# Kernel optimization log

Hardware: AMD Instinct MI355X
Metric: run time of the kernel (lower is better)

The kernel has to match this reference:

```python
import jax, jax.numpy as jnp
import numpy as np

N = 768                       # atoms
E = N * (N - 1)               # complete directed graph edges
DIM = 64                      # hidden dim
CUT = 5.0                     # rbf high
NC = 50                       # n_centers = ceil(5/0.1)
ODIM = 1                      # output_dim
NCONV = 3
_centers_np = np.linspace(0.0, CUT, NC)
CENTERS = jnp.asarray(_centers_np, jnp.float32)
GAP = float(_centers_np[1] - _centers_np[0])
RO_IN = 2 * ODIM + NC         # readout input: 2*output_dim + rbf fan_out = 52


def softplus_bt(x, beta, thr):
    # torch.nn.Softplus(beta, threshold): linear above threshold
    bx = beta * x
    return jnp.where(bx > thr, x, jax.nn.softplus(bx) / beta)


def rbf(d):
    # exp(-(1/gap) * (d - mu_k)^2); d: (..., 1) -> (..., NC)
    return jnp.exp((-1.0 / GAP) * (d - CENTERS) ** 2)


def setup_inputs() -> dict:
    key = jax.random.key(0)
    ks = jax.random.split(key, 24)
    atom_types = jax.random.randint(ks[0], (N,), 0, 100)
    edge_distances = jax.random.uniform(ks[1], (E, 1), jnp.float32) * CUT
    # complete directed graph, edge order matches the nested i,j loop (i!=j)
    ii = np.repeat(np.arange(N), N)
    jj = np.tile(np.arange(N), N)
    m = ii != jj
    src = jnp.asarray(ii[m], jnp.int32)
    dst = jnp.asarray(jj[m], jnp.int32)

    def p(k, shape, fan):
        return jax.random.normal(k, shape, jnp.float32) / np.sqrt(fan)

    embedding = p(ks[2], (100, DIM), DIM).at[0].set(0.0)  # padding_idx=0
    L = NCONV
    return {
        'atom_types': atom_types, 'edge_distances': edge_distances,
        'src': src, 'dst': dst, 'embedding': embedding,
        'w1': p(ks[3], (L, DIM, DIM), DIM),                 # node_layer1 (no bias)
        'pw1': p(ks[4], (L, NC, DIM), NC), 'pb1': p(ks[5], (L, DIM), NC),
        'pw2': p(ks[6], (L, DIM, DIM), DIM), 'pb2': p(ks[7], (L, DIM), DIM),
        'qw1': p(ks[8], (L, DIM, DIM), DIM), 'qb1': p(ks[9], (L, DIM), DIM),
        'qw2': p(ks[10], (L, DIM, DIM), DIM), 'qb2': p(ks[11], (L, DIM), DIM),
        'au_w1': p(ks[12], (DIM, 64), DIM), 'au_b1': p(ks[13], (64,), DIM),
        'au_w2': p(ks[14], (64, ODIM), 64), 'au_b2': p(ks[15], (ODIM,), 64),
        'ro_w1': p(ks[16], (RO_IN, 64), RO_IN), 'ro_b1': p(ks[17], (64,), RO_IN),
        'ro_w2': p(ks[18], (64, 2), 64), 'ro_b2': p(ks[19], (2,), 64),
    }


def reference(atom_types, edge_distances, src, dst, embedding,
              w1, pw1, pb1, pw2, pb2, qw1, qb1, qw2, qb2,
              au_w1, au_b1, au_w2, au_b2, ro_w1, ro_b1, ro_w2, ro_b2):
    h = embedding[atom_types]                       # (N, DIM)
    rbf_out = rbf(edge_distances)                   # (E, NC)
    for l in range(NCONV):
        nw = h @ w1[l]                              # node weights (N, DIM)
        e = softplus_bt(rbf_out @ pw1[l] + pb1[l], 0.5, 14) @ pw2[l] + pb2[l]  # (E, DIM)
        msg = nw[src] * e                           # gather-mul (E, DIM)
        agg = jax.ops.segment_sum(msg, dst, num_segments=N)  # scatter-sum (N, DIM)
        upd = softplus_bt(agg @ qw1[l] + qb1[l], 0.5, 14) @ qw2[l] + qb2[l]
        h = h + upd
    # atom_update with ShiftSoftplus (beta=1, shift=2, threshold=20)
    ha = softplus_bt(h @ au_w1 + au_b1, 1.0, 20) - jnp.log(jnp.float32(2.0))
    ha = ha @ au_w2 + au_b2                         # (N, ODIM)
    # readout over all ordered pairs i!=j, in edge order == (src, dst)
    edge_feat = jnp.concatenate([ha[src], ha[dst], rbf_out], axis=-1)  # (E, 52)
    logits = jax.nn.relu(edge_feat @ ro_w1 + ro_b1) @ ro_w2 + ro_b2    # (E, 2)
    return jax.nn.softmax(logits, axis=-1)
```

## Files before the change

### kernel.cpp

```cpp
#include <hip/hip_runtime.h>
#include <hip/hip_fp16.h>

#define NATOMS 768
#define NM1    767
#define NEDGE  (768*767)
#define DIM    64
#define NC     50
#define GAPF   (5.0f/49.0f)
#define NIGAP  (-49.0f/5.0f)
#define G      512
#define STEPF  (5.0f/511.0f)
#define INVSTEP (511.0f/5.0f)
#define LN2F   0.693147180559945f

#define WS_H     0
#define WS_NWA   49152
#define WS_NWB   73728
#define WS_HA    98304
#define WS_DISTT 99328
#define WS_TT    689152

__device__ __forceinline__ float softplus05(float x) {
    float bx = 0.5f * x;
    return (bx > 14.0f) ? x : 2.0f * __logf(1.0f + __expf(bx));
}
__device__ __forceinline__ int lane_bcast_i(int v, int l) {
    return __builtin_amdgcn_readlane(v, l);
}
__device__ __forceinline__ float lane_bcast_f(float v, int l) {
    return __uint_as_float((unsigned)__builtin_amdgcn_readlane((int)__float_as_uint(v), l));
}
__device__ __forceinline__ float2 pair2f(unsigned p) {
    __half2 h = *reinterpret_cast<__half2*>(&p);
    return __half22float2(h);
}

__global__ __launch_bounds__(256)
void k_pre(const int* __restrict__ types, const float* __restrict__ dist,
           const float* __restrict__ emb, const float* __restrict__ w1all,
           const float* __restrict__ pw1, const float* __restrict__ pb1,
           const float* __restrict__ pw2, const float* __restrict__ pb2,
           const float* __restrict__ row1, const float* __restrict__ rob1,
           float* __restrict__ ws) {
    __shared__ float s_t[4 * 64];
    __shared__ float s_tile[64][65];
    const int tid = threadIdx.x, widx = tid >> 6, c = tid & 63;
    float*  h     = ws + WS_H;
    __half* nwh   = (__half*)(ws + WS_NWA);
    float*  distT = ws + WS_DISTT;
    __half* TTh   = (__half*)(ws + WS_TT);
    const int b = blockIdx.x;

    if (b < 512) {
        const int w = b * 4 + widx, tbl = w >> 9, g = w & 511;
        const float d = g * STEPF;
        float val;
        if (tbl < 3) {
            const float* W1 = pw1 + tbl * NC * DIM;
            float t1 = pb1[tbl * DIM + c];
            for (int k = 0; k < NC; ++k) {
                float x = d - GAPF * (float)k;
                t1 = fmaf(__expf(NIGAP * x * x), W1[k * DIM + c], t1);
            }
            s_t[widx * 64 + c] = softplus05(t1);
            const float* W2 = pw2 + tbl * DIM * DIM;
            val = pb2[tbl * DIM + c];
            #pragma unroll 8
            for (int k = 0; k < DIM; ++k)
                val = fmaf(s_t[widx * 64 + k], W2[k * DIM + c], val);
        } else {
            val = rob1[c];
            for (int k = 0; k < NC; ++k) {
                float x = d - GAPF * (float)k;
                val = fmaf(__expf(NIGAP * x * x), row1[(2 + k) * DIM + c], val);
            }
        }
        __half* TTt = TTh + tbl * (G * DIM * 2);
        TTt[(g * DIM + c) * 2] = __float2half(val);
        if (g > 0) TTt[((g - 1) * DIM + c) * 2 + 1] = __float2half(val);
    } else if (b < 704) {
        const int i = (b - 512) * 4 + widx;
        float hv = emb[types[i] * DIM + c];
        h[i * DIM + c] = hv;
        s_t[widx * 64 + c] = hv;
        float acc = 0.0f;
        #pragma unroll 8
        for (int k = 0; k < DIM; ++k)
            acc = fmaf(s_t[widx * 64 + k], w1all[k * DIM + c], acc);
        nwh[i * 64 + c] = __float2half(acc);
    } else {
        const int t = b - 704;
        const int I0 = (t / 12) * 64, J0 = (t % 12) * 64;
        #pragma unroll 4
        for (int r = 0; r < 16; ++r) {
            const int i = I0 + widx * 16 + r;
            const int j = J0 + c;
            s_tile[widx * 16 + r][c] =
                (i == j) ? 0.0f : dist[i * NM1 + (j - (j > i))];
        }
        __syncthreads();
        #pragma unroll 4
        for (int r = 0; r < 16; ++r) {
            const int j = J0 + widx * 16 + r;
            const int i = I0 + c;
            distT[j * NATOMS + i] = s_tile[c][widx * 16 + r];
        }
    }
}

__global__ __launch_bounds__(512)
void k_edgeupd(const __half2* __restrict__ TTl, const float* __restrict__ distT,
               const __half* __restrict__ nwin,
               const float* __restrict__ qw1, const float* __restrict__ qb1,
               const float* __restrict__ qw2, const float* __restrict__ qb2,
               float* __restrict__ h,
               const float* __restrict__ wnext, __half* __restrict__ nwout,
               const float* __restrict__ auw1, const float* __restrict__ aub1,
               const float* __restrict__ auw2, const float* __restrict__ aub2,
               float* __restrict__ ha, int last) {
    __shared__ float s_part[8][64];
    __shared__ float s_upd[192];
    const int tid = threadIdx.x, widx = tid >> 6, c = tid & 63;
    const int j = blockIdx.x;
    const int s0 = widx * 96;
    const int half = c >> 5, cl = c & 31;

    const char* TTrow = (const char*)TTl + cl * 8;
    float2 csum = make_float2(0.0f, 0.0f);
    {
        float d = distT[j * NATOMS + s0 + c];
        float pos = d * INVSTEP;
        int g = (int)pos;
        g = (g < 0) ? 0 : ((g > 510) ? 510 : g);
        float f = pos - (float)g;
        int kx = g * 256;
        const char* nwrow = (const char*)nwin + s0 * 128 + half * 128 + cl * 4;
        for (int grp = 0; grp < 4; ++grp) {
            uint2 st[8]; unsigned sn[8];
            #pragma unroll
            for (int u = 0; u < 8; ++u) {
                const int t = grp * 8 + u;
                int kx0 = lane_bcast_i(kx, 2 * t);
                int kx1 = lane_bcast_i(kx, 2 * t + 1);
                int kxs = half ? kx1 : kx0;
                st[u] = *(const uint2*)(TTrow + kxs);
                sn[u] = *(const unsigned*)(nwrow + t * 256);
            }
            #pragma unroll
            for (int u = 0; u < 8; ++u) {
                const int t = grp * 8 + u;
                float f0 = lane_bcast_f(f, 2 * t);
                float f1 = lane_bcast_f(f, 2 * t + 1);
                float fs = half ? f1 : f0;
                float2 ta = pair2f(st[u].x);
                float2 tb = pair2f(st[u].y);
                float2 nwf = pair2f(sn[u]);
                float e0 = fmaf(fs, ta.y - ta.x, ta.x);
                float e1 = fmaf(fs, tb.y - tb.x, tb.x);
                csum.x = fmaf(e0, nwf.x, csum.x);
                csum.y = fmaf(e1, nwf.y, csum.y);
            }
        }
    }
    {
        float d = distT[j * NATOMS + s0 + 64 + cl];
        float pos = d * INVSTEP;
        int g = (int)pos;
        g = (g < 0) ? 0 : ((g > 510) ? 510 : g);
        float f = pos - (float)g;
        int kx = g * 256;
        const char* nwrow = (const char*)nwin + (s0 + 64) * 128 + half * 128 + cl * 4;
        for (int grp = 0; grp < 2; ++grp) {
            uint2 st[8]; unsigned sn[8];
            #pragma unroll
            for (int u = 0; u < 8; ++u) {
                const int t = grp * 8 + u;
                int kx0 = lane_bcast_i(kx, 2 * t);
                int kx1 = lane_bcast_i(kx, 2 * t + 1);
                int kxs = half ? kx1 : kx0;
                st[u] = *(const uint2*)(TTrow + kxs);
                sn[u] = *(const unsigned*)(nwrow + t * 256);
            }
            #pragma unroll
            for (int u = 0; u < 8; ++u) {
                const int t = grp * 8 + u;
                float f0 = lane_bcast_f(f, 2 * t);
                float f1 = lane_bcast_f(f, 2 * t + 1);
                float fs = half ? f1 : f0;
                float2 ta = pair2f(st[u].x);
                float2 tb = pair2f(st[u].y);
                float2 nwf = pair2f(sn[u]);
                float e0 = fmaf(fs, ta.y - ta.x, ta.x);
                float e1 = fmaf(fs, tb.y - tb.x, tb.x);
                csum.x = fmaf(e0, nwf.x, csum.x);
                csum.y = fmaf(e1, nwf.y, csum.y);
            }
        }
    }
    float2 tot2;
    tot2.x = csum.x + __shfl_xor(csum.x, 32, 64);
    tot2.y = csum.y + __shfl_xor(csum.y, 32, 64);
    if (half == 0) *(float2*)&s_part[widx][2 * cl] = tot2;
    __syncthreads();

    if (widx == 0) {
        float tot = 0.0f;
        #pragma unroll
        for (int w8 = 0; w8 < 8; ++w8) tot += s_part[w8][c];
        float2 t0 = pair2f(((const unsigned*)TTl)[c]);
        float nwj = __half2float(nwin[j * 64 + c]);
        tot -= t0.x * nwj;
        s_upd[c] = tot;
        float t = qb1[c];
        #pragma unroll 8
        for (int k = 0; k < DIM; ++k) t = fmaf(s_upd[k], qw1[k * DIM + c], t);
        s_upd[64 + c] = softplus05(t);
        float o = qb2[c];
        #pragma unroll 8
        for (int k = 0; k < DIM; ++k) o = fmaf(s_upd[64 + k], qw2[k * DIM + c], o);
        float hn = h[j * DIM + c] + o;
        h[j * DIM + c] = hn;
        s_upd[128 + c] = hn;
        if (!last) {
            float v = 0.0f;
            #pragma unroll 8
            for (int k = 0; k < DIM; ++k) v = fmaf(s_upd[128 + k], wnext[k * DIM + c], v);
            nwout[j * 64 + c] = __float2half(v);
        } else {
            float t2 = aub1[c];
            #pragma unroll 8
            for (int k = 0; k < DIM; ++k) t2 = fmaf(s_upd[128 + k], auw1[k * DIM + c], t2);
            t2 = ((t2 > 20.0f) ? t2 : __logf(1.0f + __expf(t2))) - LN2F;
            float v = t2 * auw2[c];
            #pragma unroll
            for (int s = 32; s > 0; s >>= 1) v += __shfl_down(v, s, 64);
            if (c == 0) ha[j] = v + aub2[0];
        }
    }
}

__global__ __launch_bounds__(256)
void k_ro(const float* __restrict__ dist, const float* __restrict__ ha,
          const __half2* __restrict__ TTro,
          const float* __restrict__ row1, const float* __restrict__ row2,
          const float* __restrict__ rob2, float* __restrict__ out) {
    __shared__ float s_h[4][16 * 65];
    __shared__ float s_w2[128];
    const int tid = threadIdx.x, widx = tid >> 6, c = tid & 63;
    if (tid < 128) s_w2[tid] = row2[tid];
    __syncthreads();
    const int ebase = (blockIdx.x * 4 + widx) * 64;

    int kxv; float ff, fa, fb;
    {
        int eg = ebase + c;
        float d = dist[eg];
        float pos = d * INVSTEP;
        int kk = (int)pos;
        kk = (kk < 0) ? 0 : ((kk > 510) ? 510 : kk);
        kxv = kk * 256;
        ff = pos - (float)kk;
        unsigned i = (unsigned)(((unsigned long long)(unsigned)eg * 2867044662ull) >> 41);
        int r = eg - (int)i * 767;
        int jd = r + (r >= (int)i);
        fa = ha[i];
        fb = ha[jd];
    }
    const char* TTb2 = (const char*)TTro + c * 4;
    const float wa = row1[c], wb = row1[DIM + c];
    const int e2 = (c >> 1) & 15, p2 = c & 1, kh = c >> 5;
    const float bias2 = (kh == 0) ? rob2[p2] : 0.0f;
    float* sh = s_h[widx];
    #pragma unroll
    for (int ch = 0; ch < 4; ++ch) {
        #pragma unroll
        for (int half = 0; half < 2; ++half) {
            unsigned st[8];
            #pragma unroll
            for (int u = 0; u < 8; ++u) {
                const int le = ch * 16 + half * 8 + u;
                int kxu = lane_bcast_i(kxv, le);
                st[u] = *(const unsigned*)(TTb2 + kxu);
            }
            #pragma unroll
            for (int u = 0; u < 8; ++u) {
                const int le = ch * 16 + half * 8 + u;
                const int e = half * 8 + u;
                float fu  = lane_bcast_f(ff, le);
                float fau = lane_bcast_f(fa, le);
                float fbu = lane_bcast_f(fb, le);
                float2 tt = pair2f(st[u]);
                float hv = fmaf(fu, tt.y - tt.x, tt.x);
                hv = fmaf(fau, wa, hv);
                hv = fmaf(fbu, wb, hv);
                sh[e * 65 + c] = fmaxf(hv, 0.0f);
            }
        }
        float lsum = bias2;
        #pragma unroll 8
        for (int k8 = 0; k8 < 32; ++k8) {
            int k = kh * 32 + k8;
            lsum = fmaf(sh[e2 * 65 + k], s_w2[2 * k + p2], lsum);
        }
        lsum += __shfl_xor(lsum, 32, 64);
        float other = __shfl_xor(lsum, 1, 64);
        float m = fmaxf(lsum, other);
        float ea = __expf(lsum - m), eb = __expf(other - m);
        float r = ea / (ea + eb);
        if (c < 32) out[ebase * 2 + ch * 32 + c] = r;
    }
}

extern "C" void kernel_launch(void* const* d_in, const int* in_sizes, int n_in,
                              void* d_out, int out_size, void* d_ws, size_t ws_size,
                              hipStream_t stream) {
    const int*   types = (const int*)d_in[0];
    const float* dist  = (const float*)d_in[1];
    const float* emb   = (const float*)d_in[4];
    const float* w1    = (const float*)d_in[5];
    const float* pw1   = (const float*)d_in[6];
    const float* pb1   = (const float*)d_in[7];
    const float* pw2   = (const float*)d_in[8];
    const float* pb2   = (const float*)d_in[9];
    const float* qw1   = (const float*)d_in[10];
    const float* qb1   = (const float*)d_in[11];
    const float* qw2   = (const float*)d_in[12];
    const float* qb2   = (const float*)d_in[13];
    const float* auw1  = (const float*)d_in[14];
    const float* aub1  = (const float*)d_in[15];
    const float* auw2  = (const float*)d_in[16];
    const float* aub2  = (const float*)d_in[17];
    const float* row1  = (const float*)d_in[18];
    const float* rob1  = (const float*)d_in[19];
    const float* row2  = (const float*)d_in[20];
    const float* rob2  = (const float*)d_in[21];

    float* ws   = (float*)d_ws;
    float* outp = (float*)d_out;
    const __half2* TT = (const __half2*)(ws + WS_TT);
    __half* nwbuf[2] = { (__half*)(ws + WS_NWA), (__half*)(ws + WS_NWB) };

    k_pre<<<848, 256, 0, stream>>>(types, dist, emb, w1, pw1, pb1, pw2, pb2,
                                   row1, rob1, ws);
    for (int l = 0; l < 3; ++l) {
        k_edgeupd<<<768, 512, 0, stream>>>(TT + l * (G * DIM),
            ws + WS_DISTT, nwbuf[l & 1],
            qw1 + l * DIM * DIM, qb1 + l * DIM,
            qw2 + l * DIM * DIM, qb2 + l * DIM,
            ws + WS_H,
            (l < 2) ? (w1 + (l + 1) * DIM * DIM) : w1, nwbuf[(l + 1) & 1],
            auw1, aub1, auw2, aub2, ws + WS_HA, (l == 2) ? 1 : 0);
    }
    k_ro<<<2301, 256, 0, stream>>>(dist, ws + WS_HA, TT + 3 * (G * DIM),
                                   row1, row2, rob2, outp);
}
```

Measured before the change: 181.2 us.

## Sort incoming edges by distance bin per destination to improve table locality

The preprocessing kernel now counting-sorts each destination's 768 incoming edges by their RBF lookup bin, storing the sorted position key and source index, instead of building a transposed distance matrix. The edge-update kernel then reads sorted keys and gathers node weights indirectly through the source index. Neighbouring lanes therefore hit nearby rows of the interpolation table, which should improve cache locality for the table fetches. In exchange the node-weight loads become gathers and k_pre does extra histogram, scan and atomic work.

Measured after the change: 191.3 us. 1.06x slower.

```diff
diff --git a/kernel.cpp b/kernel.cpp
--- a/kernel.cpp
+++ b/kernel.cpp
@@ -17,8 +17,9 @@
 #define WS_NWA   49152
 #define WS_NWB   73728
 #define WS_HA    98304
-#define WS_DISTT 99328
+#define WS_SKEY  99328
 #define WS_TT    689152
+#define WS_SSRC  820224
 
 __device__ __forceinline__ float softplus05(float x) {
     float bx = 0.5f * x;
@@ -43,11 +44,14 @@
            const float* __restrict__ row1, const float* __restrict__ rob1,
            float* __restrict__ ws) {
     __shared__ float s_t[4 * 64];
-    __shared__ float s_tile[64][65];
+    __shared__ int s_hist[512];
+    __shared__ int s_base[512];
+    __shared__ int s_scan[256];
     const int tid = threadIdx.x, widx = tid >> 6, c = tid & 63;
     float*  h     = ws + WS_H;
     __half* nwh   = (__half*)(ws + WS_NWA);
-    float*  distT = ws + WS_DISTT;
+    float*  skey  = ws + WS_SKEY;
+    int*    ssrc  = (int*)(ws + WS_SSRC);
     __half* TTh   = (__half*)(ws + WS_TT);
     const int b = blockIdx.x;
 
@@ -89,28 +93,49 @@
             acc = fmaf(s_t[widx * 64 + k], w1all[k * DIM + c], acc);
         nwh[i * 64 + c] = __float2half(acc);
     } else {
-        const int t = b - 704;
-        const int I0 = (t / 12) * 64, J0 = (t % 12) * 64;
-        #pragma unroll 4
-        for (int r = 0; r < 16; ++r) {
-            const int i = I0 + widx * 16 + r;
-            const int j = J0 + c;
-            s_tile[widx * 16 + r][c] =
-                (i == j) ? 0.0f : dist[i * NM1 + (j - (j > i))];
-        }
+        const int j = b - 704;
+        s_hist[tid] = 0; s_hist[tid + 256] = 0;
         __syncthreads();
-        #pragma unroll 4
-        for (int r = 0; r < 16; ++r) {
-            const int j = J0 + widx * 16 + r;
-            const int i = I0 + c;
-            distT[j * NATOMS + i] = s_tile[c][widx * 16 + r];
+        float p_[3]; int g_[3];
+        #pragma unroll
+        for (int r = 0; r < 3; ++r) {
+            const int i = tid + r * 256;
+            float d = (i == j) ? 0.0f : dist[i * NM1 + (j - (j > i))];
+            float pos = d * INVSTEP;
+            int g = (int)pos;
+            g = (g < 0) ? 0 : ((g > 510) ? 510 : g);
+            p_[r] = pos; g_[r] = g;
+            atomicAdd(&s_hist[g], 1);
+        }
+        __syncthreads();
+        int a0 = s_hist[2 * tid], a1 = s_hist[2 * tid + 1];
+        s_scan[tid] = a0 + a1;
+        __syncthreads();
+        for (int off = 1; off < 256; off <<= 1) {
+            int v = s_scan[tid];
+            int w = (tid >= off) ? s_scan[tid - off] : 0;
+            __syncthreads();
+            s_scan[tid] = v + w;
+            __syncthreads();
+        }
+        int ex = (tid > 0) ? s_scan[tid - 1] : 0;
+        s_base[2 * tid] = ex;
+        s_base[2 * tid + 1] = ex + a0;
+        s_hist[2 * tid] = 0; s_hist[2 * tid + 1] = 0;
+        __syncthreads();
+        #pragma unroll
+        for (int r = 0; r < 3; ++r) {
+            const int i = tid + r * 256;
+            int slot = s_base[g_[r]] + atomicAdd(&s_hist[g_[r]], 1);
+            skey[j * NATOMS + slot] = p_[r];
+            ssrc[j * NATOMS + slot] = i;
         }
     }
 }
 
 __global__ __launch_bounds__(512)
-void k_edgeupd(const __half2* __restrict__ TTl, const float* __restrict__ distT,
-               const __half* __restrict__ nwin,
+void k_edgeupd(const __half2* __restrict__ TTl, const float* __restrict__ skey,
+               const int* __restrict__ ssrc, const __half* __restrict__ nwin,
                const float* __restrict__ qw1, const float* __restrict__ qb1,
                const float* __restrict__ qw2, const float* __restrict__ qb2,
                float* __restrict__ h,
@@ -126,15 +151,15 @@
     const int half = c >> 5, cl = c & 31;
 
     const char* TTrow = (const char*)TTl + cl * 8;
+    const char* nwl   = (const char*)nwin + cl * 4;
     float2 csum = make_float2(0.0f, 0.0f);
     {
-        float d = distT[j * NATOMS + s0 + c];
-        float pos = d * INVSTEP;
+        float pos = skey[j * NATOMS + s0 + c];
+        int nwo = ssrc[j * NATOMS + s0 + c] << 7;
         int g = (int)pos;
         g = (g < 0) ? 0 : ((g > 510) ? 510 : g);
         float f = pos - (float)g;
         int kx = g * 256;
-        const char* nwrow = (const char*)nwin + s0 * 128 + half * 128 + cl * 4;
         for (int grp = 0; grp < 4; ++grp) {
             uint2 st[8]; unsigned sn[8];
             #pragma unroll
@@ -142,9 +167,12 @@
                 const int t = grp * 8 + u;
                 int kx0 = lane_bcast_i(kx, 2 * t);
                 int kx1 = lane_bcast_i(kx, 2 * t + 1);
+                int no0 = lane_bcast_i(nwo, 2 * t);
+                int no1 = lane_bcast_i(nwo, 2 * t + 1);
                 int kxs = half ? kx1 : kx0;
+                int nos = half ? no1 : no0;
                 st[u] = *(const uint2*)(TTrow + kxs);
-                sn[u] = *(const unsigned*)(nwrow + t * 256);
+                sn[u] = *(const unsigned*)(nwl + nos);
             }
             #pragma unroll
             for (int u = 0; u < 8; ++u) {
@@ -163,13 +191,12 @@
         }
     }
     {
-        float d = distT[j * NATOMS + s0 + 64 + cl];
-        float pos = d * INVSTEP;
+        float pos = skey[j * NATOMS + s0 + 64 + cl];
+        int nwo = ssrc[j * NATOMS + s0 + 64 + cl] << 7;
         int g = (int)pos;
         g = (g < 0) ? 0 : ((g > 510) ? 510 : g);
         float f = pos - (float)g;
         int kx = g * 256;
-        const char* nwrow = (const char*)nwin + (s0 + 64) * 128 + half * 128 + cl * 4;
         for (int grp = 0; grp < 2; ++grp) {
             uint2 st[8]; unsigned sn[8];
             #pragma unroll
@@ -177,9 +204,12 @@
                 const int t = grp * 8 + u;
                 int kx0 = lane_bcast_i(kx, 2 * t);
                 int kx1 = lane_bcast_i(kx, 2 * t + 1);
+                int no0 = lane_bcast_i(nwo, 2 * t);
+                int no1 = lane_bcast_i(nwo, 2 * t + 1);
                 int kxs = half ? kx1 : kx0;
+                int nos = half ? no1 : no0;
                 st[u] = *(const uint2*)(TTrow + kxs);
-                sn[u] = *(const unsigned*)(nwrow + t * 256);
+                sn[u] = *(const unsigned*)(nwl + nos);
             }
             #pragma unroll
             for (int u = 0; u < 8; ++u) {
@@ -340,11 +370,11 @@
     const __half2* TT = (const __half2*)(ws + WS_TT);
     __half* nwbuf[2] = { (__half*)(ws + WS_NWA), (__half*)(ws + WS_NWB) };
 
-    k_pre<<<848, 256, 0, stream>>>(types, dist, emb, w1, pw1, pb1, pw2, pb2,
-                                   row1, rob1, ws);
+    k_pre<<<1472, 256, 0, stream>>>(types, dist, emb, w1, pw1, pb1, pw2, pb2,
+                                    row1, rob1, ws);
     for (int l = 0; l < 3; ++l) {
         k_edgeupd<<<768, 512, 0, stream>>>(TT + l * (G * DIM),
-            ws + WS_DISTT, nwbuf[l & 1],
+            ws + WS_SKEY, (const int*)(ws + WS_SSRC), nwbuf[l & 1],
             qw1 + l * DIM * DIM, qb1 + l * DIM,
             qw2 + l * DIM * DIM, qb2 + l * DIM,
             ws + WS_H,
```
